# Kernel tuning notes

Measured on AMD Instinct MI355X. Metric: run time of the kernel, lower is better.

## Reference

```python
import jax, jax.numpy as jnp
import numpy as np

WS = 8        # window_size
SHIFT = 4     # shift_size
NH = 6        # num_heads
EPS = 1e-5


def _rel_pos_index(ws):
    coords = np.stack(np.meshgrid(np.arange(ws), np.arange(ws), indexing='ij'))  # [2,ws,ws]
    cf = coords.reshape(2, -1)                      # [2, ws*ws]
    rel = cf[:, :, None] - cf[:, None, :]           # [2, N, N]
    rel = rel.transpose(1, 2, 0)                    # [N, N, 2]
    rel[:, :, 0] += ws - 1
    rel[:, :, 1] += ws - 1
    rel[:, :, 0] *= 2 * ws - 1
    return rel.sum(-1)                              # [N, N] int


def _attn_mask(H, W, ws, shift):
    img = np.zeros((H, W), dtype=np.float32)
    slices = (slice(0, -ws), slice(-ws, -shift), slice(-shift, None))
    cnt = 0
    for hs in slices:
        for wsl in slices:
            img[hs, wsl] = cnt
            cnt += 1
    mw = img.reshape(H // ws, ws, W // ws, ws).transpose(0, 2, 1, 3).reshape(-1, ws * ws)
    diff = mw[:, None, :] - mw[:, :, None]          # [nW, N, N]
    return np.where(diff != 0, -100.0, 0.0).astype(np.float32)


def _layernorm(x, g, b):
    mu = x.mean(-1, keepdims=True)
    var = ((x - mu) ** 2).mean(-1, keepdims=True)
    return (x - mu) * jax.lax.rsqrt(var + EPS) * g + b


def setup_inputs() -> dict:
    key = jax.random.key(0)
    ks = jax.random.split(key, 8)
    C, HID = 192, 768
    return {
        'x': jax.random.normal(ks[0], (8, 128, 128, C), jnp.float32),
        'g1': jnp.ones((C,), jnp.float32),
        'b1': jnp.zeros((C,), jnp.float32),
        'qkv_w': jax.random.normal(ks[1], (3 * C, C), jnp.float32) * 0.02,
        'qkv_b': jnp.zeros((3 * C,), jnp.float32),
        'rpb_table': jax.random.normal(ks[2], ((2 * WS - 1) ** 2, NH), jnp.float32) * 0.02,
        'proj_w': jax.random.normal(ks[3], (C, C), jnp.float32) * 0.02,
        'proj_b': jnp.zeros((C,), jnp.float32),
        'g2': jnp.ones((C,), jnp.float32),
        'b2': jnp.zeros((C,), jnp.float32),
        'fc1_w': jax.random.normal(ks[4], (HID, C), jnp.float32) * 0.02,
        'fc1_b': jnp.zeros((HID,), jnp.float32),
        'fc2_w': jax.random.normal(ks[5], (C, HID), jnp.float32) * 0.02,
        'fc2_b': jnp.zeros((C,), jnp.float32),
    }


def reference(x, g1, b1, qkv_w, qkv_b, rpb_table, proj_w, proj_b, g2, b2,
              fc1_w, fc1_b, fc2_w, fc2_b):
    B, H, W, C = x.shape
    N = WS * WS
    hd = C // NH
    scale = hd ** -0.5

    rpi = jnp.asarray(_rel_pos_index(WS))                 # [N,N] static
    mask = jnp.asarray(_attn_mask(H, W, WS, SHIFT))       # [nW,N,N] static
    nW = mask.shape[0]

    shortcut = x.reshape(B, H * W, C)
    xn = _layernorm(shortcut, g1, b1).reshape(B, H, W, C)

    # cyclic shift
    xs = jnp.roll(xn, shift=(-SHIFT, -SHIFT), axis=(1, 2))

    # window partition -> [B*nW, N, C]
    win = xs.reshape(B, H // WS, WS, W // WS, WS, C).transpose(0, 1, 3, 2, 4, 5)
    win = win.reshape(-1, N, C)
    B_ = win.shape[0]

    # qkv
    qkv = jnp.einsum('bnc,oc->bno', win, qkv_w) + qkv_b   # [B_,N,3C]
    qkv = qkv.reshape(B_, N, 3, NH, hd).transpose(2, 0, 3, 1, 4)  # [3,B_,NH,N,hd]
    q, k, v = qkv[0] * scale, qkv[1], qkv[2]

    attn = jnp.einsum('bhnd,bhmd->bhnm', q, k)            # [B_,NH,N,N]
    bias = rpb_table[rpi.reshape(-1)].reshape(N, N, NH).transpose(2, 0, 1)
    attn = attn + bias[None]
    attn = attn.reshape(B, nW, NH, N, N) + mask[None, :, None]
    attn = jax.nn.softmax(attn.reshape(B_, NH, N, N), axis=-1)

    out = jnp.einsum('bhnm,bhmd->bhnd', attn, v)          # [B_,NH,N,hd]
    out = out.transpose(0, 2, 1, 3).reshape(B_, N, C)
    out = jnp.einsum('bnc,oc->bno', out, proj_w) + proj_b

    # window reverse -> [B,H,W,C]
    out = out.reshape(B, H // WS, W // WS, WS, WS, C).transpose(0, 1, 3, 2, 4, 5)
    out = out.reshape(B, H, W, C)
    out = jnp.roll(out, shift=(SHIFT, SHIFT), axis=(1, 2)).reshape(B, H * W, C)

    x1 = shortcut + out
    h = _layernorm(x1, g2, b2)
    h = jnp.einsum('bnc,hc->bnh', h, fc1_w) + fc1_b
    h = jax.nn.gelu(h, approximate=False)
    h = jnp.einsum('bnh,ch->bnc', h, fc2_w) + fc2_b
    x2 = x1 + h
    return x2.reshape(B, H, W, C)
```

## Files before the change

### kernel.cpp

```cpp
#include <hip/hip_runtime.h>
#include <hip/hip_bf16.h>

typedef __attribute__((ext_vector_type(8))) short s16x8;
typedef __attribute__((ext_vector_type(4))) float f32x4;

__device__ __forceinline__ unsigned short f2bf(float f){
    __hip_bfloat16 h = __float2bfloat16(f);
    return *reinterpret_cast<unsigned short*>(&h);
}

__device__ __forceinline__ int flab(int g){ return (g < 120) ? 0 : ((g < 124) ? 1 : 2); }

__device__ __forceinline__ void async16(const void* g, void* l){
    __builtin_amdgcn_global_load_lds(
        (const __attribute__((address_space(1))) unsigned int*)g,
        (__attribute__((address_space(3))) unsigned int*)l, 16, 0, 0);
}

__global__ __launch_bounds__(256) void wconv_all(
    const float* __restrict__ w0, const float* __restrict__ w1,
    const float* __restrict__ w2, const float* __restrict__ w3,
    unsigned short* __restrict__ o0, unsigned short* __restrict__ o1,
    unsigned short* __restrict__ o2, unsigned short* __restrict__ o3)
{
    int i = blockIdx.x*256 + threadIdx.x;
    if (i < 110592) o0[i] = f2bf(w0[i]);
    if (i < 36864)  o1[i] = f2bf(w1[i]);
    if (i < 147456) o2[i] = f2bf(w2[i]);
    if (i < 147456) o3[i] = f2bf(w3[i]);
}

__global__ __launch_bounds__(256) void lnqkv_kernel(
    const float* __restrict__ x, const float* __restrict__ g1, const float* __restrict__ b1,
    const unsigned short* __restrict__ wq, const float* __restrict__ qkvb,
    unsigned short* __restrict__ qo, unsigned short* __restrict__ ko,
    unsigned short* __restrict__ vo)
{
    __shared__ __attribute__((aligned(16))) unsigned short win[64*200];
    __shared__ __attribute__((aligned(16))) unsigned short Bs[64*200];
    const int b_ = blockIdx.x;
    const int bb = b_>>8, wi = b_&255, wh = wi>>4, ww = wi&15;
    const int tid = threadIdx.x;
    const int wv = tid>>6, lane = tid&63, lrow = lane&15, quad = lane>>4;

    {
        const int n = tid>>2, q4 = tid&3;
        const int r = n>>3, c = n&7;
        const int hh = (wh*8 + r + 4)&127, wp = (ww*8 + c + 4)&127;
        const float* px = x + (((size_t)bb*128+hh)*128+wp)*192 + q4*48;
        float v[48];
        #pragma unroll
        for (int m=0;m<12;++m) *(float4*)(v+m*4) = *(const float4*)(px+m*4);
        float s = 0.f;
        #pragma unroll
        for (int k=0;k<48;++k) s += v[k];
        s += __shfl_xor(s,1); s += __shfl_xor(s,2);
        float mu = s*(1.0f/192.0f);
        float qv = 0.f;
        #pragma unroll
        for (int k=0;k<48;++k){ float d=v[k]-mu; qv += d*d; }
        qv += __shfl_xor(qv,1); qv += __shfl_xor(qv,2);
        float rstd = rsqrtf(qv*(1.0f/192.0f) + 1e-5f);
        const float* pg = g1 + q4*48;
        const float* pb = b1 + q4*48;
        unsigned short* pw = win + n*200 + q4*48;
        #pragma unroll
        for (int k=0;k<48;++k) pw[k] = f2bf((v[k]-mu)*rstd*pg[k] + pb[k]);
    }
    __syncthreads();

    s16x8 af[6];
    #pragma unroll
    for (int kc=0;kc<6;++kc)
        af[kc] = *(const s16x8*)(win + (wv*16+lrow)*200 + kc*32 + quad*8);

    for (int ot=0; ot<9; ++ot) {
        const int o0 = ot*64;
        __syncthreads();
        #pragma unroll
        for (int t=0;t<6;++t) {
            int cid = tid + t*256;
            *(int4*)(Bs + (cid/24)*200 + (cid%24)*8) =
                *(const int4*)(wq + (size_t)o0*192 + cid*8);
        }
        __syncthreads();
        f32x4 acc[4];
        #pragma unroll
        for (int j=0;j<4;++j) acc[j] = (f32x4){0.f,0.f,0.f,0.f};
        #pragma unroll
        for (int kc=0;kc<6;++kc)
            #pragma unroll
            for (int j=0;j<4;++j) {
                s16x8 bf = *(const s16x8*)(Bs + (j*16+lrow)*200 + kc*32 + quad*8);
                acc[j] = __builtin_amdgcn_mfma_f32_16x16x32_bf16(af[kc], bf, acc[j], 0, 0, 0);
            }
        __syncthreads();
        unsigned short* T = Bs;
        const int part = ot/3;
        float bv[4];
        #pragma unroll
        for (int j=0;j<4;++j) bv[j] = qkvb[o0 + j*16 + lrow];

        if (part < 2) {
            const float scale = (part==0) ? 0.17677669529663687f : 1.0f;
            #pragma unroll
            for (int j=0;j<4;++j)
                #pragma unroll
                for (int rg=0;rg<4;++rg) {
                    int n2 = wv*16 + quad*4 + rg;
                    T[n2*72 + j*16 + lrow] = f2bf((acc[j][rg]+bv[j])*scale);
                }
            __syncthreads();
            unsigned short* dst = (part==0) ? qo : ko;
            #pragma unroll
            for (int t=0;t<2;++t) {
                int c = tid + t*256;
                int n2 = c>>3, blk = c&7;
                int o_in = o0 + blk*8 - part*192;
                int head = o_in>>5, d = o_in&31;
                *(int4*)(dst + (((size_t)b_*6+head)*64 + n2)*32 + d) =
                    *(const int4*)(T + n2*72 + blk*8);
            }
        } else {
            #pragma unroll
            for (int j=0;j<4;++j)
                #pragma unroll
                for (int rg=0;rg<4;++rg) {
                    int n2 = wv*16 + quad*4 + rg;
                    T[(j*16+lrow)*72 + n2] = f2bf(acc[j][rg]+bv[j]);
                }
            __syncthreads();
            #pragma unroll
            for (int t=0;t<2;++t) {
                int c = tid + t*256;
                int ol = c>>3, nb = (c&7)*8;
                int o_in = o0 + ol - 384;
                int head = o_in>>5, d = o_in&31;
                *(int4*)(vo + (((size_t)b_*6+head)*32 + d)*64 + nb) =
                    *(const int4*)(T + ol*72 + nb);
            }
        }
    }
}

__global__ __launch_bounds__(384) void attn_kernel(
    const unsigned short* __restrict__ q, const unsigned short* __restrict__ k,
    const unsigned short* __restrict__ vT, const float* __restrict__ rpb,
    unsigned short* __restrict__ ao)
{
    __shared__ float rpb_s[1350];
    __shared__ __attribute__((aligned(16))) unsigned short p_lds[6*4608];
    const int b_ = blockIdx.x;
    const int h = threadIdx.x >> 6;
    const int lane = threadIdx.x & 63, lrow = lane & 15, quad = lane >> 4;
    for (int i = threadIdx.x; i < 1350; i += 384) rpb_s[i] = rpb[i];
    __syncthreads();

    const size_t hb = ((size_t)b_*6 + h)*2048;
    const unsigned short* qb = q  + hb;
    const unsigned short* kb = k  + hb;
    const unsigned short* vb = vT + hb;

    s16x8 qf[4], kf[4];
    #pragma unroll
    for (int i = 0; i < 4; ++i) qf[i] = *(const s16x8*)(qb + (i*16+lrow)*32 + quad*8);
    #pragma unroll
    for (int j = 0; j < 4; ++j) kf[j] = *(const s16x8*)(kb + (j*16+lrow)*32 + quad*8);

    const f32x4 zz = {0.f,0.f,0.f,0.f};
    f32x4 s[4][4];
    #pragma unroll
    for (int i = 0; i < 4; ++i)
        #pragma unroll
        for (int j = 0; j < 4; ++j)
            s[i][j] = __builtin_amdgcn_mfma_f32_16x16x32_bf16(qf[i], kf[j], zz, 0, 0, 0);

    const int wi = b_ & 255, wh = wi >> 4, ww = wi & 15;
    int labm[4];
    #pragma unroll
    for (int j = 0; j < 4; ++j) {
        int m = j*16 + lrow;
        labm[j] = flab(wh*8 + (m >> 3))*3 + flab(ww*8 + (m & 7));
    }
    unsigned short* pl = p_lds + h*4608;
    #pragma unroll
    for (int i = 0; i < 4; ++i) {
        #pragma unroll
        for (int rg = 0; rg < 4; ++rg) {
            int n = i*16 + quad*4 + rg;
            int rn = n >> 3, cn = n & 7;
            int labn = flab(wh*8 + rn)*3 + flab(ww*8 + cn);
            float vals[4];
            float vmax = -1e30f;
            #pragma unroll
            for (int j = 0; j < 4; ++j) {
                int m = j*16 + lrow;
                int idx = ((rn - (m >> 3) + 7)*15 + (cn - (m & 7) + 7))*6 + h;
                float val = s[i][j][rg] + rpb_s[idx];
                if (labn != labm[j]) val -= 100.f;
                vals[j] = val;
                vmax = fmaxf(vmax, val);
            }
            #pragma unroll
            for (int o = 1; o < 16; o <<= 1) vmax = fmaxf(vmax, __shfl_xor(vmax, o));
            float sum = 0.f;
            #pragma unroll
            for (int j = 0; j < 4; ++j) { vals[j] = __expf(vals[j] - vmax); sum += vals[j]; }
            #pragma unroll
            for (int o = 1; o < 16; o <<= 1) sum += __shfl_xor(sum, o);
            float inv = 1.f / sum;
            #pragma unroll
            for (int j = 0; j < 4; ++j) pl[n*72 + j*16 + lrow] = f2bf(vals[j]*inv);
        }
    }
    __syncthreads();

    f32x4 oacc[4][2];
    #pragma unroll
    for (int i = 0; i < 4; ++i) { oacc[i][0] = zz; oacc[i][1] = zz; }
    #pragma unroll
    for (int kc = 0; kc < 2; ++kc) {
        s16x8 vf[2];
        #pragma unroll
        for (int jd = 0; jd < 2; ++jd)
            vf[jd] = *(const s16x8*)(vb + (jd*16+lrow)*64 + kc*32 + quad*8);
        #pragma unroll
        for (int i = 0; i < 4; ++i) {
            s16x8 pf = *(const s16x8*)(pl + (i*16+lrow)*72 + kc*32 + quad*8);
            #pragma unroll
            for (int jd = 0; jd < 2; ++jd)
                oacc[i][jd] = __builtin_amdgcn_mfma_f32_16x16x32_bf16(pf, vf[jd], oacc[i][jd], 0, 0, 0);
        }
    }
    unsigned short* ob = ao + (size_t)b_*12288 + h*32;
    #pragma unroll
    for (int i = 0; i < 4; ++i)
        #pragma unroll
        for (int jd = 0; jd < 2; ++jd)
            #pragma unroll
            for (int rg = 0; rg < 4; ++rg) {
                int n = i*16 + quad*4 + rg;
                ob[(size_t)n*192 + jd*16 + lrow] = f2bf(oacc[i][jd][rg]);
            }
}

__global__ __launch_bounds__(256) void projln_kernel(
    const unsigned short* __restrict__ A, const unsigned short* __restrict__ W,
    const float* __restrict__ pbias, const float* __restrict__ x,
    const float* __restrict__ g2, const float* __restrict__ b2,
    float* __restrict__ x1, unsigned short* __restrict__ xln2)
{
    __shared__ __attribute__((aligned(16))) char smem[36864];
    unsigned short* As = (unsigned short*)smem;
    unsigned short* Bs = (unsigned short*)(smem + 9216);
    const int b_ = blockIdx.x;
    const int tid = threadIdx.x, wv = tid>>6, lane = tid&63;
    const int lrow = lane&15, quad = lane>>4;
    const size_t m0 = (size_t)b_*64;

    f32x4 acc[12];
    #pragma unroll
    for (int j=0;j<12;++j) acc[j] = (f32x4){0.f,0.f,0.f,0.f};

    for (int k0=0;k0<192;k0+=64) {
        __syncthreads();
        #pragma unroll
        for (int t=0;t<2;++t) {
            int cid = tid + t*256;
            *(int4*)(As + (cid>>3)*72 + (cid&7)*8) =
                *(const int4*)(A + (m0 + (cid>>3))*192 + k0 + (cid&7)*8);
        }
        #pragma unroll
        for (int t=0;t<6;++t) {
            int cid = tid + t*256;
            *(int4*)(Bs + (cid>>3)*72 + (cid&7)*8) =
                *(const int4*)(W + (size_t)(cid>>3)*192 + k0 + (cid&7)*8);
        }
        __syncthreads();
        #pragma unroll
        for (int kc=0;kc<2;++kc) {
            s16x8 af = *(const s16x8*)(As + (wv*16+lrow)*72 + kc*32 + quad*8);
            #pragma unroll
            for (int j=0;j<12;++j) {
                s16x8 bf = *(const s16x8*)(Bs + (j*16+lrow)*72 + kc*32 + quad*8);
                acc[j] = __builtin_amdgcn_mfma_f32_16x16x32_bf16(af, bf, acc[j], 0, 0, 0);
            }
        }
    }
    __syncthreads();

    const int bb = b_>>8, wi = b_&255, wh = wi>>4, ww = wi&15;
    float bv[12], gv[12], b2v[12];
    #pragma unroll
    for (int j=0;j<12;++j) {
        bv[j]  = pbias[j*16+lrow];
        gv[j]  = g2[j*16+lrow];
        b2v[j] = b2[j*16+lrow];
    }
    unsigned short* T = (unsigned short*)smem;
    #pragma unroll
    for (int rg=0;rg<4;++rg) {
        int n2 = wv*16 + quad*4 + rg;
        int r = n2>>3, c = n2&7;
        int hh = (wh*8+r+4)&127, wp = (ww*8+c+4)&127;
        size_t tok = ((size_t)bb*128+hh)*128 + wp;
        float xv[12];
        float s = 0.f;
        #pragma unroll
        for (int j=0;j<12;++j) {
            float t = acc[j][rg] + bv[j] + x[tok*192 + j*16 + lrow];
            xv[j] = t; s += t;
        }
        #pragma unroll
        for (int o=1;o<16;o<<=1) s += __shfl_xor(s, o);
        float mu = s*(1.0f/192.0f);
        float qv = 0.f;
        #pragma unroll
        for (int j=0;j<12;++j){ float d = xv[j]-mu; qv += d*d; }
        #pragma unroll
        for (int o=1;o<16;o<<=1) qv += __shfl_xor(qv, o);
        float rstd = rsqrtf(qv*(1.0f/192.0f) + 1e-5f);
        #pragma unroll
        for (int j=0;j<12;++j) {
            x1[tok*192 + j*16 + lrow] = xv[j];
            T[n2*200 + j*16 + lrow] = f2bf((xv[j]-mu)*rstd*gv[j] + b2v[j]);
        }
    }
    __syncthreads();
    #pragma unroll
    for (int t=0;t<6;++t) {
        int cid = tid + t*256;
        int n2 = cid/24, blk = cid%24;
        int r = n2>>3, c = n2&7;
        int hh = (wh*8+r+4)&127, wp = (ww*8+c+4)&127;
        size_t tok = ((size_t)bb*128+hh)*128 + wp;
        *(int4*)(xln2 + tok*192 + blk*8) = *(const int4*)(T + n2*200 + blk*8);
    }
}

__device__ __forceinline__ void mm128x64(
    const unsigned short* __restrict__ A, const unsigned short* __restrict__ W,
    int K, size_t m0, int o0, unsigned short* As, unsigned short* Bs,
    f32x4 (&acc)[2][4])
{
    const int tid = threadIdx.x, wv = tid>>6, lane = tid&63;
    const int lrow = lane&15, quad = lane>>4;
    const int lr8 = lane>>3, lb = lane&7;
    const int sb = ((lb ^ lr8) << 3);
    #pragma unroll
    for (int i=0;i<2;++i)
        #pragma unroll
        for (int j=0;j<4;++j) acc[i][j] = (f32x4){0.f,0.f,0.f,0.f};

    const unsigned short* Abase = A + (m0 + wv*8 + lr8)*K + sb;
    const unsigned short* Wbase = W + (size_t)(o0 + wv*8 + lr8)*K + sb;

    for (int k0=0;k0<K;k0+=64) {
        #pragma unroll
        for (int it=0;it<4;++it)
            async16(Abase + (size_t)(it*32)*K + k0, As + (it*4+wv)*512);
        #pragma unroll
        for (int it=0;it<2;++it)
            async16(Wbase + (size_t)(it*32)*K + k0, Bs + (it*4+wv)*512);
        __syncthreads();
        #pragma unroll
        for (int kc=0;kc<2;++kc) {
            const int blk = quad + 4*kc;
            s16x8 af[2], bf[4];
            #pragma unroll
            for (int i=0;i<2;++i) {
                int row = wv*32 + i*16 + lrow;
                af[i] = *(const s16x8*)(As + row*64 + ((blk ^ (row&7)) << 3));
            }
            #pragma unroll
            for (int j=0;j<4;++j) {
                int row = j*16 + lrow;
                bf[j] = *(const s16x8*)(Bs + row*64 + ((blk ^ (row&7)) << 3));
            }
            #pragma unroll
            for (int i=0;i<2;++i)
                #pragma unroll
                for (int j=0;j<4;++j)
                    acc[i][j] = __builtin_amdgcn_mfma_f32_16x16x32_bf16(af[i], bf[j], acc[i][j], 0, 0, 0);
        }
        __syncthreads();
    }
}

__global__ __launch_bounds__(256) void gemm_fc1_kernel(
    const unsigned short* __restrict__ A, const unsigned short* __restrict__ Wm,
    const float* __restrict__ bias, unsigned short* __restrict__ h1)
{
    __shared__ __attribute__((aligned(16))) char smem[24576];
    unsigned short* As = (unsigned short*)smem;
    unsigned short* Bs = (unsigned short*)(smem + 16384);
    const size_t m0 = (size_t)blockIdx.y*128;
    const int o0 = blockIdx.x*64;
    f32x4 acc[2][4];
    mm128x64(A, Wm, 192, m0, o0, As, Bs, acc);
    const int tid = threadIdx.x, wv = tid>>6, lane = tid&63;
    const int lrow = lane&15, quad = lane>>4;
    float bv[4];
    #pragma unroll
    for (int j=0;j<4;++j) bv[j] = bias[o0 + j*16 + lrow];
    unsigned short* T = (unsigned short*)smem;
    #pragma unroll
    for (int i=0;i<2;++i)
        #pragma unroll
        for (int j=0;j<4;++j)
            #pragma unroll
            for (int rg=0;rg<4;++rg) {
                int ml = wv*32 + i*16 + quad*4 + rg;
                float v = acc[i][j][rg] + bv[j];
                v = 0.5f*v*(1.0f + erff(v*0.7071067811865475f));
                T[ml*72 + j*16 + lrow] = f2bf(v);
            }
    __syncthreads();
    #pragma unroll
    for (int t=0;t<4;++t) {
        int c = tid + t*256;
        int row = c>>3, blk = c&7;
        *(int4*)(h1 + (m0+row)*768 + o0 + blk*8) = *(const int4*)(T + row*72 + blk*8);
    }
}

__global__ __launch_bounds__(256) void gemm_fc2_kernel(
    const unsigned short* __restrict__ A, const unsigned short* __restrict__ Wm,
    const float* __restrict__ bias, const float* __restrict__ x1, float* __restrict__ out)
{
    __shared__ __attribute__((aligned(16))) char smem[24576];
    unsigned short* As = (unsigned short*)smem;
    unsigned short* Bs = (unsigned short*)(smem + 16384);
    const size_t m0 = (size_t)blockIdx.y*128;
    const int o0 = blockIdx.x*64;
    f32x4 acc[2][4];
    mm128x64(A, Wm, 768, m0, o0, As, Bs, acc);
    const int tid = threadIdx.x, wv = tid>>6, lane = tid&63;
    const int lrow = lane&15, quad = lane>>4;
    float bv[4];
    #pragma unroll
    for (int j=0;j<4;++j) bv[j] = bias[o0 + j*16 + lrow];
    float* T = (float*)smem;
    #pragma unroll
    for (int p=0;p<2;++p) {
        __syncthreads();
        if ((wv>>1) == p) {
            int wl = wv&1;
            #pragma unroll
            for (int i=0;i<2;++i)
                #pragma unroll
                for (int j=0;j<4;++j)
                    #pragma unroll
                    for (int rg=0;rg<4;++rg)
                        T[(wl*32 + i*16 + quad*4 + rg)*68 + j*16 + lrow] = acc[i][j][rg] + bv[j];
        }
        __syncthreads();
        #pragma unroll
        for (int t=0;t<4;++t) {
            int c = tid + t*256;
            int row = c>>4, blk = c&15;
            size_t ad = (m0 + p*64 + row)*192 + o0 + blk*4;
            float4 v = *(const float4*)(T + row*68 + blk*4);
            float4 rx = *(const float4*)(x1 + ad);
            v.x += rx.x; v.y += rx.y; v.z += rx.z; v.w += rx.w;
            *(float4*)(out + ad) = v;
        }
    }
}

extern "C" void kernel_launch(void* const* d_in, const int* in_sizes, int n_in,
                              void* d_out, int out_size, void* d_ws, size_t ws_size,
                              hipStream_t stream)
{
    const float* x      = (const float*)d_in[0];
    const float* g1     = (const float*)d_in[1];
    const float* b1     = (const float*)d_in[2];
    const float* qkv_w  = (const float*)d_in[3];
    const float* qkv_b  = (const float*)d_in[4];
    const float* rpb    = (const float*)d_in[5];
    const float* proj_w = (const float*)d_in[6];
    const float* proj_b = (const float*)d_in[7];
    const float* g2     = (const float*)d_in[8];
    const float* b2     = (const float*)d_in[9];
    const float* fc1_w  = (const float*)d_in[10];
    const float* fc1_b  = (const float*)d_in[11];
    const float* fc2_w  = (const float*)d_in[12];
    const float* fc2_b  = (const float*)d_in[13];
    float* out = (float*)d_out;
    char* ws = (char*)d_ws;

    if (ws_size < 353206272ULL) return;

    unsigned short* qbuf  = (unsigned short*)(ws + 0);
    unsigned short* kbuf  = (unsigned short*)(ws + 50331648);
    unsigned short* vbuf  = (unsigned short*)(ws + 100663296);
    unsigned short* attnO = (unsigned short*)(ws + 150994944);
    float*          x1    = (float*)        (ws + 201326592);
    unsigned short* xln2  = (unsigned short*)(ws + 301989888);
    unsigned short* wq    = (unsigned short*)(ws + 352321536);
    unsigned short* wp    = (unsigned short*)(ws + 352321536 + 221184);
    unsigned short* w1    = (unsigned short*)(ws + 352321536 + 221184 + 73728);
    unsigned short* w2    = (unsigned short*)(ws + 352321536 + 221184 + 73728 + 294912);
    unsigned short* h1    = (unsigned short*)(ws + 0);

    wconv_all<<<576, 256, 0, stream>>>(qkv_w, proj_w, fc1_w, fc2_w, wq, wp, w1, w2);
    lnqkv_kernel<<<2048, 256, 0, stream>>>(x, g1, b1, wq, qkv_b, qbuf, kbuf, vbuf);
    attn_kernel<<<2048, 384, 0, stream>>>(qbuf, kbuf, vbuf, rpb, attnO);
    projln_kernel<<<2048, 256, 0, stream>>>(attnO, wp, proj_b, x, g2, b2, x1, xln2);
    gemm_fc1_kernel<<<dim3(12, 1024), 256, 0, stream>>>(xln2, w1, fc1_b, h1);
    gemm_fc2_kernel<<<dim3(3, 1024), 256, 0, stream>>>(h1, w2, fc2_b, x1, out);
}
```

Before: 595.9 us.

## Widen MLP GEMM tiles to 128x192 and double-buffer LDS K-loop

The shared GEMM helper now computes 128x192 output tiles instead of 128x64 and keeps two LDS buffers, so the loads for the next K-slice are issued while the current one is being multiplied, with one barrier per step. The fc2 GEMM covers all 192 output columns in a single block, so each h1 row tile is read once rather than three times. fc1 uses 4 column blocks instead of 12, which cuts repeated A reads. The cost is 80KB of LDS per block and 96 accumulator registers per lane, which limits occupancy (launch bounds ask for 2 blocks per CU), and the fc1 grid becomes smaller.

```diff
diff --git a/kernel.cpp b/kernel.cpp
--- a/kernel.cpp
+++ b/kernel.cpp
@@ -338,10 +338,11 @@
     }
 }
 
-__device__ __forceinline__ void mm128x64(
+template<int K>
+__device__ __forceinline__ void mm128x192(
     const unsigned short* __restrict__ A, const unsigned short* __restrict__ W,
-    int K, size_t m0, int o0, unsigned short* As, unsigned short* Bs,
-    f32x4 (&acc)[2][4])
+    size_t m0, int o0, unsigned short* As, unsigned short* Bs,
+    f32x4 (&acc)[2][12])
 {
     const int tid = threadIdx.x, wv = tid>>6, lane = tid&63;
     const int lrow = lane&15, quad = lane>>4;
@@ -350,96 +351,108 @@
     #pragma unroll
     for (int i=0;i<2;++i)
         #pragma unroll
-        for (int j=0;j<4;++j) acc[i][j] = (f32x4){0.f,0.f,0.f,0.f};
+        for (int j=0;j<12;++j) acc[i][j] = (f32x4){0.f,0.f,0.f,0.f};
 
     const unsigned short* Abase = A + (m0 + wv*8 + lr8)*K + sb;
     const unsigned short* Wbase = W + (size_t)(o0 + wv*8 + lr8)*K + sb;
 
-    for (int k0=0;k0<K;k0+=64) {
-        #pragma unroll
-        for (int it=0;it<4;++it)
-            async16(Abase + (size_t)(it*32)*K + k0, As + (it*4+wv)*512);
-        #pragma unroll
-        for (int it=0;it<2;++it)
-            async16(Wbase + (size_t)(it*32)*K + k0, Bs + (it*4+wv)*512);
-        __syncthreads();
+    #pragma unroll
+    for (int it=0;it<4;++it) async16(Abase + (size_t)(it*32)*K, As + (it*4+wv)*512);
+    #pragma unroll
+    for (int it=0;it<6;++it) async16(Wbase + (size_t)(it*32)*K, Bs + (it*4+wv)*512);
+
+    int cur = 0;
+    for (int k0=0; k0<K; k0+=64) {
+        __syncthreads();
+        if (k0 + 64 < K) {
+            unsigned short* An = As + (cur^1)*8192;
+            unsigned short* Bn = Bs + (cur^1)*12288;
+            #pragma unroll
+            for (int it=0;it<4;++it)
+                async16(Abase + (size_t)(it*32)*K + (k0+64), An + (it*4+wv)*512);
+            #pragma unroll
+            for (int it=0;it<6;++it)
+                async16(Wbase + (size_t)(it*32)*K + (k0+64), Bn + (it*4+wv)*512);
+        }
+        const unsigned short* Ac = As + cur*8192;
+        const unsigned short* Bc = Bs + cur*12288;
         #pragma unroll
         for (int kc=0;kc<2;++kc) {
             const int blk = quad + 4*kc;
-            s16x8 af[2], bf[4];
+            s16x8 af[2], bf[12];
             #pragma unroll
             for (int i=0;i<2;++i) {
                 int row = wv*32 + i*16 + lrow;
-                af[i] = *(const s16x8*)(As + row*64 + ((blk ^ (row&7)) << 3));
-            }
-            #pragma unroll
-            for (int j=0;j<4;++j) {
+                af[i] = *(const s16x8*)(Ac + row*64 + ((blk ^ (row&7)) << 3));
+            }
+            #pragma unroll
+            for (int j=0;j<12;++j) {
                 int row = j*16 + lrow;
-                bf[j] = *(const s16x8*)(Bs + row*64 + ((blk ^ (row&7)) << 3));
+                bf[j] = *(const s16x8*)(Bc + row*64 + ((blk ^ (row&7)) << 3));
             }
             #pragma unroll
             for (int i=0;i<2;++i)
                 #pragma unroll
-                for (int j=0;j<4;++j)
+                for (int j=0;j<12;++j)
                     acc[i][j] = __builtin_amdgcn_mfma_f32_16x16x32_bf16(af[i], bf[j], acc[i][j], 0, 0, 0);
         }
-        __syncthreads();
-    }
-}
-
-__global__ __launch_bounds__(256) void gemm_fc1_kernel(
+        cur ^= 1;
+    }
+}
+
+__global__ __launch_bounds__(256, 2) void gemm_fc1_kernel(
     const unsigned short* __restrict__ A, const unsigned short* __restrict__ Wm,
     const float* __restrict__ bias, unsigned short* __restrict__ h1)
 {
-    __shared__ __attribute__((aligned(16))) char smem[24576];
+    __shared__ __attribute__((aligned(16))) char smem[81920];
     unsigned short* As = (unsigned short*)smem;
-    unsigned short* Bs = (unsigned short*)(smem + 16384);
+    unsigned short* Bs = (unsigned short*)(smem + 32768);
     const size_t m0 = (size_t)blockIdx.y*128;
-    const int o0 = blockIdx.x*64;
-    f32x4 acc[2][4];
-    mm128x64(A, Wm, 192, m0, o0, As, Bs, acc);
+    const int o0 = blockIdx.x*192;
+    f32x4 acc[2][12];
+    mm128x192<192>(A, Wm, m0, o0, As, Bs, acc);
     const int tid = threadIdx.x, wv = tid>>6, lane = tid&63;
     const int lrow = lane&15, quad = lane>>4;
-    float bv[4];
-    #pragma unroll
-    for (int j=0;j<4;++j) bv[j] = bias[o0 + j*16 + lrow];
+    float bv[12];
+    #pragma unroll
+    for (int j=0;j<12;++j) bv[j] = bias[o0 + j*16 + lrow];
+    __syncthreads();
     unsigned short* T = (unsigned short*)smem;
     #pragma unroll
     for (int i=0;i<2;++i)
         #pragma unroll
-        for (int j=0;j<4;++j)
+        for (int j=0;j<12;++j)
             #pragma unroll
             for (int rg=0;rg<4;++rg) {
                 int ml = wv*32 + i*16 + quad*4 + rg;
                 float v = acc[i][j][rg] + bv[j];
                 v = 0.5f*v*(1.0f + erff(v*0.7071067811865475f));
-                T[ml*72 + j*16 + lrow] = f2bf(v);
-            }
-    __syncthreads();
-    #pragma unroll
-    for (int t=0;t<4;++t) {
+                T[ml*200 + j*16 + lrow] = f2bf(v);
+            }
+    __syncthreads();
+    #pragma unroll
+    for (int t=0;t<12;++t) {
         int c = tid + t*256;
-        int row = c>>3, blk = c&7;
-        *(int4*)(h1 + (m0+row)*768 + o0 + blk*8) = *(const int4*)(T + row*72 + blk*8);
-    }
-}
-
-__global__ __launch_bounds__(256) void gemm_fc2_kernel(
+        int row = c/24, blk = c%24;
+        *(int4*)(h1 + (m0+row)*768 + o0 + blk*8) = *(const int4*)(T + row*200 + blk*8);
+    }
+}
+
+__global__ __launch_bounds__(256, 2) void gemm_fc2_kernel(
     const unsigned short* __restrict__ A, const unsigned short* __restrict__ Wm,
     const float* __restrict__ bias, const float* __restrict__ x1, float* __restrict__ out)
 {
-    __shared__ __attribute__((aligned(16))) char smem[24576];
+    __shared__ __attribute__((aligned(16))) char smem[81920];
     unsigned short* As = (unsigned short*)smem;
-    unsigned short* Bs = (unsigned short*)(smem + 16384);
-    const size_t m0 = (size_t)blockIdx.y*128;
-    const int o0 = blockIdx.x*64;
-    f32x4 acc[2][4];
-    mm128x64(A, Wm, 768, m0, o0, As, Bs, acc);
+    unsigned short* Bs = (unsigned short*)(smem + 32768);
+    const size_t m0 = (size_t)blockIdx.x*128;
+    f32x4 acc[2][12];
+    mm128x192<768>(A, Wm, m0, 0, As, Bs, acc);
     const int tid = threadIdx.x, wv = tid>>6, lane = tid&63;
     const int lrow = lane&15, quad = lane>>4;
-    float bv[4];
-    #pragma unroll
-    for (int j=0;j<4;++j) bv[j] = bias[o0 + j*16 + lrow];
+    float bv[12];
+    #pragma unroll
+    for (int j=0;j<12;++j) bv[j] = bias[j*16 + lrow];
     float* T = (float*)smem;
     #pragma unroll
     for (int p=0;p<2;++p) {
@@ -449,18 +462,18 @@
             #pragma unroll
             for (int i=0;i<2;++i)
                 #pragma unroll
-                for (int j=0;j<4;++j)
+                for (int j=0;j<12;++j)
                     #pragma unroll
                     for (int rg=0;rg<4;++rg)
-                        T[(wl*32 + i*16 + quad*4 + rg)*68 + j*16 + lrow] = acc[i][j][rg] + bv[j];
-        }
-        __syncthreads();
-        #pragma unroll
-        for (int t=0;t<4;++t) {
+                        T[(wl*32 + i*16 + quad*4 + rg)*196 + j*16 + lrow] = acc[i][j][rg] + bv[j];
+        }
+        __syncthreads();
+        #pragma unroll
+        for (int t=0;t<12;++t) {
             int c = tid + t*256;
-            int row = c>>4, blk = c&15;
-            size_t ad = (m0 + p*64 + row)*192 + o0 + blk*4;
-            float4 v = *(const float4*)(T + row*68 + blk*4);
+            int row = c/48, blk = c%48;
+            size_t ad = (m0 + p*64 + row)*192 + blk*4;
+            float4 v = *(const float4*)(T + row*196 + blk*4);
             float4 rx = *(const float4*)(x1 + ad);
             v.x += rx.x; v.y += rx.y; v.z += rx.z; v.w += rx.w;
             *(float4*)(out + ad) = v;
@@ -507,6 +520,6 @@
     lnqkv_kernel<<<2048, 256, 0, stream>>>(x, g1, b1, wq, qkv_b, qbuf, kbuf, vbuf);
     attn_kernel<<<2048, 384, 0, stream>>>(qbuf, kbuf, vbuf, rpb, attnO);
     projln_kernel<<<2048, 256, 0, stream>>>(attnO, wp, proj_b, x, g2, b2, x1, xln2);
-    gemm_fc1_kernel<<<dim3(12, 1024), 256, 0, stream>>>(xln2, w1, fc1_b, h1);
-    gemm_fc2_kernel<<<dim3(3, 1024), 256, 0, stream>>>(h1, w2, fc2_b, x1, out);
-}
+    gemm_fc1_kernel<<<dim3(4, 1024), 256, 0, stream>>>(xln2, w1, fc1_b, h1);
+    gemm_fc2_kernel<<<1024, 256, 0, stream>>>(h1, w2, fc2_b, x1, out);
+}
```

New measurement: 579.5 us. 2.8% less time.

## Retile MLP GEMMs to 128x96 with double-buffered K=32 stages and block swizzle

Applied to the files above, without the earlier changes.

Replaces the 128x64 tile GEMM with a 128x96 tile that runs over K in steps of 32, using double-buffered LDS and async global-to-LDS prefetch of the next stage. Block indices are remapped through a swizzle so that neighbouring blocks share A rows, and launch bounds now request higher occupancy. The exact erf GELU in fc1 is swapped for a tanh-form sigmoid approximation built on exp and a fast reciprocal. The aim is fewer redundant A loads, memory latency hidden behind compute, and a cheaper epilogue, at some cost in GELU accuracy.

```diff
diff --git a/kernel.cpp b/kernel.cpp
--- a/kernel.cpp
+++ b/kernel.cpp
@@ -338,108 +338,130 @@
     }
 }
 
-__device__ __forceinline__ void mm128x64(
+__device__ __forceinline__ void mm128x96(
     const unsigned short* __restrict__ A, const unsigned short* __restrict__ W,
     int K, size_t m0, int o0, unsigned short* As, unsigned short* Bs,
-    f32x4 (&acc)[2][4])
+    f32x4 (&acc)[2][6])
 {
     const int tid = threadIdx.x, wv = tid>>6, lane = tid&63;
     const int lrow = lane&15, quad = lane>>4;
-    const int lr8 = lane>>3, lb = lane&7;
-    const int sb = ((lb ^ lr8) << 3);
+    const int lr4 = lane>>2, lc4 = lane&3;
+    const int cb = lc4 ^ (lr4&3);
     #pragma unroll
     for (int i=0;i<2;++i)
         #pragma unroll
-        for (int j=0;j<4;++j) acc[i][j] = (f32x4){0.f,0.f,0.f,0.f};
-
-    const unsigned short* Abase = A + (m0 + wv*8 + lr8)*K + sb;
-    const unsigned short* Wbase = W + (size_t)(o0 + wv*8 + lr8)*K + sb;
-
-    for (int k0=0;k0<K;k0+=64) {
-        #pragma unroll
-        for (int it=0;it<4;++it)
-            async16(Abase + (size_t)(it*32)*K + k0, As + (it*4+wv)*512);
-        #pragma unroll
-        for (int it=0;it<2;++it)
-            async16(Wbase + (size_t)(it*32)*K + k0, Bs + (it*4+wv)*512);
-        __syncthreads();
-        #pragma unroll
-        for (int kc=0;kc<2;++kc) {
-            const int blk = quad + 4*kc;
-            s16x8 af[2], bf[4];
-            #pragma unroll
-            for (int i=0;i<2;++i) {
-                int row = wv*32 + i*16 + lrow;
-                af[i] = *(const s16x8*)(As + row*64 + ((blk ^ (row&7)) << 3));
-            }
-            #pragma unroll
-            for (int j=0;j<4;++j) {
-                int row = j*16 + lrow;
-                bf[j] = *(const s16x8*)(Bs + row*64 + ((blk ^ (row&7)) << 3));
-            }
-            #pragma unroll
-            for (int i=0;i<2;++i)
-                #pragma unroll
-                for (int j=0;j<4;++j)
-                    acc[i][j] = __builtin_amdgcn_mfma_f32_16x16x32_bf16(af[i], bf[j], acc[i][j], 0, 0, 0);
-        }
-        __syncthreads();
-    }
-}
-
-__global__ __launch_bounds__(256) void gemm_fc1_kernel(
+        for (int j=0;j<6;++j) acc[i][j] = (f32x4){0.f,0.f,0.f,0.f};
+
+    const unsigned short* Abase = A + (m0 + lr4)*(size_t)K + cb*8;
+    const unsigned short* Wbase = W + ((size_t)(o0 + lr4))*K + cb*8;
+
+    #pragma unroll
+    for (int it=0;it<2;++it) {
+        int ia = wv + it*4;
+        async16(Abase + (size_t)(ia*16)*K, As + ia*512);
+    }
+    #pragma unroll
+    for (int it=0;it<2;++it) {
+        int ib = wv + it*4;
+        if (ib < 6) async16(Wbase + (size_t)(ib*16)*K, Bs + ib*512);
+    }
+
+    int cur = 0;
+    for (int k0=0; k0<K; k0+=32) {
+        __syncthreads();
+        if (k0 + 32 < K) {
+            unsigned short* An = As + (cur^1)*4096;
+            unsigned short* Bn = Bs + (cur^1)*3072;
+            #pragma unroll
+            for (int it=0;it<2;++it) {
+                int ia = wv + it*4;
+                async16(Abase + (size_t)(ia*16)*K + (k0+32), An + ia*512);
+            }
+            #pragma unroll
+            for (int it=0;it<2;++it) {
+                int ib = wv + it*4;
+                if (ib < 6) async16(Wbase + (size_t)(ib*16)*K + (k0+32), Bn + ib*512);
+            }
+        }
+        const unsigned short* Ac = As + cur*4096;
+        const unsigned short* Bc = Bs + cur*3072;
+        const int rs = (quad ^ (lrow&3)) << 3;
+        s16x8 af[2], bf[6];
+        #pragma unroll
+        for (int i=0;i<2;++i)
+            af[i] = *(const s16x8*)(Ac + (wv*32 + i*16 + lrow)*32 + rs);
+        #pragma unroll
+        for (int j=0;j<6;++j)
+            bf[j] = *(const s16x8*)(Bc + (j*16 + lrow)*32 + rs);
+        #pragma unroll
+        for (int i=0;i<2;++i)
+            #pragma unroll
+            for (int j=0;j<6;++j)
+                acc[i][j] = __builtin_amdgcn_mfma_f32_16x16x32_bf16(af[i], bf[j], acc[i][j], 0, 0, 0);
+        cur ^= 1;
+    }
+}
+
+__global__ __launch_bounds__(256, 4) void gemm_fc1_kernel(
     const unsigned short* __restrict__ A, const unsigned short* __restrict__ Wm,
     const float* __restrict__ bias, unsigned short* __restrict__ h1)
 {
-    __shared__ __attribute__((aligned(16))) char smem[24576];
+    __shared__ __attribute__((aligned(16))) char smem[28672];
     unsigned short* As = (unsigned short*)smem;
     unsigned short* Bs = (unsigned short*)(smem + 16384);
-    const size_t m0 = (size_t)blockIdx.y*128;
-    const int o0 = blockIdx.x*64;
-    f32x4 acc[2][4];
-    mm128x64(A, Wm, 192, m0, o0, As, Bs, acc);
+    const int bid = blockIdx.x;
+    const int virt = (bid & 7)*1024 + (bid >> 3);
+    const size_t m0 = (size_t)(virt >> 3)*128;
+    const int o0 = (virt & 7)*96;
+    f32x4 acc[2][6];
+    mm128x96(A, Wm, 192, m0, o0, As, Bs, acc);
     const int tid = threadIdx.x, wv = tid>>6, lane = tid&63;
     const int lrow = lane&15, quad = lane>>4;
-    float bv[4];
-    #pragma unroll
-    for (int j=0;j<4;++j) bv[j] = bias[o0 + j*16 + lrow];
+    float bv[6];
+    #pragma unroll
+    for (int j=0;j<6;++j) bv[j] = bias[o0 + j*16 + lrow];
+    __syncthreads();
     unsigned short* T = (unsigned short*)smem;
     #pragma unroll
     for (int i=0;i<2;++i)
         #pragma unroll
-        for (int j=0;j<4;++j)
+        for (int j=0;j<6;++j)
             #pragma unroll
             for (int rg=0;rg<4;++rg) {
                 int ml = wv*32 + i*16 + quad*4 + rg;
                 float v = acc[i][j][rg] + bv[j];
-                v = 0.5f*v*(1.0f + erff(v*0.7071067811865475f));
-                T[ml*72 + j*16 + lrow] = f2bf(v);
-            }
-    __syncthreads();
-    #pragma unroll
-    for (int t=0;t<4;++t) {
+                float v2 = v*v;
+                float z = v*(1.5957691216057308f + 0.07135481627f*v2);
+                float r = v * __builtin_amdgcn_rcpf(1.f + __expf(-z));
+                T[ml*104 + j*16 + lrow] = f2bf(r);
+            }
+    __syncthreads();
+    #pragma unroll
+    for (int t=0;t<6;++t) {
         int c = tid + t*256;
-        int row = c>>3, blk = c&7;
-        *(int4*)(h1 + (m0+row)*768 + o0 + blk*8) = *(const int4*)(T + row*72 + blk*8);
-    }
-}
-
-__global__ __launch_bounds__(256) void gemm_fc2_kernel(
+        int row = c/12, blk = c%12;
+        *(int4*)(h1 + (m0+row)*768 + o0 + blk*8) = *(const int4*)(T + row*104 + blk*8);
+    }
+}
+
+__global__ __launch_bounds__(256, 4) void gemm_fc2_kernel(
     const unsigned short* __restrict__ A, const unsigned short* __restrict__ Wm,
     const float* __restrict__ bias, const float* __restrict__ x1, float* __restrict__ out)
 {
-    __shared__ __attribute__((aligned(16))) char smem[24576];
+    __shared__ __attribute__((aligned(16))) char smem[28672];
     unsigned short* As = (unsigned short*)smem;
     unsigned short* Bs = (unsigned short*)(smem + 16384);
-    const size_t m0 = (size_t)blockIdx.y*128;
-    const int o0 = blockIdx.x*64;
-    f32x4 acc[2][4];
-    mm128x64(A, Wm, 768, m0, o0, As, Bs, acc);
+    const int bid = blockIdx.x;
+    const int virt = (bid & 7)*256 + (bid >> 3);
+    const size_t m0 = (size_t)(virt >> 1)*128;
+    const int o0 = (virt & 1)*96;
+    f32x4 acc[2][6];
+    mm128x96(A, Wm, 768, m0, o0, As, Bs, acc);
     const int tid = threadIdx.x, wv = tid>>6, lane = tid&63;
     const int lrow = lane&15, quad = lane>>4;
-    float bv[4];
-    #pragma unroll
-    for (int j=0;j<4;++j) bv[j] = bias[o0 + j*16 + lrow];
+    float bv[6];
+    #pragma unroll
+    for (int j=0;j<6;++j) bv[j] = bias[o0 + j*16 + lrow];
     float* T = (float*)smem;
     #pragma unroll
     for (int p=0;p<2;++p) {
@@ -449,18 +471,18 @@
             #pragma unroll
             for (int i=0;i<2;++i)
                 #pragma unroll
-                for (int j=0;j<4;++j)
+                for (int j=0;j<6;++j)
                     #pragma unroll
                     for (int rg=0;rg<4;++rg)
-                        T[(wl*32 + i*16 + quad*4 + rg)*68 + j*16 + lrow] = acc[i][j][rg] + bv[j];
-        }
-        __syncthreads();
-        #pragma unroll
-        for (int t=0;t<4;++t) {
+                        T[(wl*32 + i*16 + quad*4 + rg)*100 + j*16 + lrow] = acc[i][j][rg] + bv[j];
+        }
+        __syncthreads();
+        #pragma unroll
+        for (int t=0;t<6;++t) {
             int c = tid + t*256;
-            int row = c>>4, blk = c&15;
+            int row = c/24, blk = c%24;
             size_t ad = (m0 + p*64 + row)*192 + o0 + blk*4;
-            float4 v = *(const float4*)(T + row*68 + blk*4);
+            float4 v = *(const float4*)(T + row*100 + blk*4);
             float4 rx = *(const float4*)(x1 + ad);
             v.x += rx.x; v.y += rx.y; v.z += rx.z; v.w += rx.w;
             *(float4*)(out + ad) = v;
@@ -507,6 +529,6 @@
     lnqkv_kernel<<<2048, 256, 0, stream>>>(x, g1, b1, wq, qkv_b, qbuf, kbuf, vbuf);
     attn_kernel<<<2048, 384, 0, stream>>>(qbuf, kbuf, vbuf, rpb, attnO);
     projln_kernel<<<2048, 256, 0, stream>>>(attnO, wp, proj_b, x, g2, b2, x1, xln2);
-    gemm_fc1_kernel<<<dim3(12, 1024), 256, 0, stream>>>(xln2, w1, fc1_b, h1);
-    gemm_fc2_kernel<<<dim3(3, 1024), 256, 0, stream>>>(h1, w2, fc2_b, x1, out);
-}
+    gemm_fc1_kernel<<<8192, 256, 0, stream>>>(xln2, w1, fc1_b, h1);
+    gemm_fc2_kernel<<<2048, 256, 0, stream>>>(h1, w2, fc2_b, x1, out);
+}
```

Result: faster. 566.5 us (-4.9%).
